# Performance work log

Hardware: AMD Instinct MI355X
Metric: run time of the kernel (lower is better)

Reference implementation:

```python
import jax, jax.numpy as jnp
import numpy as np

B, S, H, OUT = 512, 128, 512, 1
IN = 1
P = 0.1  # drop_rate


def setup_inputs() -> dict:
    key = jax.random.key(0)
    ks = jax.random.split(key, 14)
    x = jax.random.normal(ks[0], (B, S), dtype=jnp.float32)
    # Bayesian LSTM variational params (blitz-style: W = mu + log1p(exp(rho)) * eps)
    W_ih_mu = jax.random.normal(ks[1], (IN, 4 * H), dtype=jnp.float32) * 0.1
    W_ih_rho = jnp.full((IN, 4 * H), -5.0, dtype=jnp.float32)
    eps_ih = jax.random.normal(ks[2], (IN, 4 * H), dtype=jnp.float32)
    W_hh_mu = jax.random.normal(ks[3], (H, 4 * H), dtype=jnp.float32) * 0.1
    W_hh_rho = jnp.full((H, 4 * H), -5.0, dtype=jnp.float32)
    eps_hh = jax.random.normal(ks[4], (H, 4 * H), dtype=jnp.float32)
    b_mu = jax.random.normal(ks[5], (4 * H,), dtype=jnp.float32) * 0.1
    b_rho = jnp.full((4 * H,), -5.0, dtype=jnp.float32)
    eps_b = jax.random.normal(ks[6], (4 * H,), dtype=jnp.float32)
    # linear head
    W_lin = jax.random.normal(ks[7], (H, OUT), dtype=jnp.float32) * 0.05
    b_lin = jnp.zeros((OUT,), dtype=jnp.float32)
    # dropout masks (training=True always); pre-scaled inverted dropout
    keep = 1.0 - P
    mask_in = jax.random.bernoulli(ks[8], keep, (B, S, 1)).astype(jnp.float32) / keep
    # second dropout is applied to hidden_seq then sliced at t=-1, so only the
    # last-step mask matters
    mask_out = jax.random.bernoulli(ks[9], keep, (B, H)).astype(jnp.float32) / keep
    return {
        "x": x,
        "W_ih_mu": W_ih_mu, "W_ih_rho": W_ih_rho, "eps_ih": eps_ih,
        "W_hh_mu": W_hh_mu, "W_hh_rho": W_hh_rho, "eps_hh": eps_hh,
        "b_mu": b_mu, "b_rho": b_rho, "eps_b": eps_b,
        "W_lin": W_lin, "b_lin": b_lin,
        "mask_in": mask_in, "mask_out": mask_out,
    }


def reference(x, W_ih_mu, W_ih_rho, eps_ih, W_hh_mu, W_hh_rho, eps_hh,
              b_mu, b_rho, eps_b, W_lin, b_lin, mask_in, mask_out):
    # reparameterized weight samples
    W_ih = W_ih_mu + jnp.log1p(jnp.exp(W_ih_rho)) * eps_ih   # (IN, 4H)
    W_hh = W_hh_mu + jnp.log1p(jnp.exp(W_hh_rho)) * eps_hh   # (H, 4H)
    b = b_mu + jnp.log1p(jnp.exp(b_rho)) * eps_b             # (4H,)

    # reshape (B,S) -> (B,S,1) + input dropout
    xr = x[:, :, None] * mask_in                              # (B,S,1)
    # input projection for all timesteps at once
    x_proj = jnp.einsum('bsi,ih->bsh', xr, W_ih) + b          # (B,S,4H)
    xs = jnp.swapaxes(x_proj, 0, 1)                           # (S,B,4H)

    h0 = jnp.zeros((B, H), dtype=x.dtype)
    c0 = jnp.zeros((B, H), dtype=x.dtype)

    def step(carry, gx):
        h, c = carry
        gates = gx + h @ W_hh                                 # (B,4H)
        i_g, f_g, g_g, o_g = jnp.split(gates, 4, axis=-1)
        i_t = jax.nn.sigmoid(i_g)
        f_t = jax.nn.sigmoid(f_g)
        g_t = jnp.tanh(g_g)
        o_t = jax.nn.sigmoid(o_g)
        c_new = f_t * c + i_t * g_t
        h_new = o_t * jnp.tanh(c_new)
        return (h_new, c_new), h_new

    (h_last, _), _ = jax.lax.scan(step, (h0, c0), xs)
    # output dropout (only last step matters after slicing), then linear head
    out = (h_last * mask_out) @ W_lin + b_lin                 # (B,OUT)
    return out
```

## Files before the change

kernel.cpp:

```cpp
#include <hip/hip_runtime.h>
#include <hip/hip_bf16.h>


typedef __attribute__((ext_vector_type(8))) _Float16 half8;
typedef __attribute__((ext_vector_type(4))) float f32x4;
typedef unsigned long long u64;
typedef unsigned int u32;

#define HID   512
#define BATCH 512
#define SEQ   128

__device__ __forceinline__ float bf2f(__hip_bfloat16 v) { return __bfloat162float(v); }
__device__ __forceinline__ float softplus_f(float x) { return log1pf(__expf(x)); }
__device__ __forceinline__ float sigm(float x) { return 1.f / (1.f + __expf(-x)); }
__device__ __forceinline__ float tanh_fast(float x) {
  x = fminf(fmaxf(x, -15.f), 15.f);
  float e = __expf(2.f * x);
  return (e - 1.f) / (e + 1.f);
}
__device__ __forceinline__ float ldin(const void* p, size_t i, int md) {
  return md ? ((const float*)p)[i] : bf2f(((const __hip_bfloat16*)p)[i]);
}
__device__ __forceinline__ unsigned short f16bits(_Float16 h) {
  union { _Float16 f; unsigned short u; } c; c.f = h; return c.u;
}
__device__ __forceinline__ u64 ald64(const u64* p) {
  return __hip_atomic_load((u64*)p, __ATOMIC_RELAXED, __HIP_MEMORY_SCOPE_AGENT);
}
__device__ __forceinline__ u32 ald32(const u32* p) {
  return __hip_atomic_load((u32*)p, __ATOMIC_RELAXED, __HIP_MEMORY_SCOPE_AGENT);
}
__device__ __forceinline__ void ast32(u32* p, u32 v) {
  (void)__hip_atomic_exchange(p, v, __ATOMIC_RELAXED, __HIP_MEMORY_SCOPE_AGENT);
}
__device__ __forceinline__ void ast64(u64* p, u64 v) {
  (void)__hip_atomic_exchange(p, v, __ATOMIC_RELAXED, __HIP_MEMORY_SCOPE_AGENT);
}

__global__ void detect_mode(const u32* __restrict__ rho_bits, int* __restrict__ mode) {
  *mode = (rho_bits[0] == 0xC0A00000u) ? 1 : 0;
}

__global__ __launch_bounds__(256) void setup_weights(
    const void* __restrict__ mu, const void* __restrict__ rho,
    const void* __restrict__ eps, unsigned short* __restrict__ Wtf,
    const int* __restrict__ mode) {
  const int md = *mode;
  const int idx = blockIdx.x * 256 + threadIdx.x;
  const int k = idx >> 11, ncol = idx & 2047;
  const float w = ldin(mu, idx, md) + softplus_f(ldin(rho, idx, md)) * ldin(eps, idx, md);
  const int g = ncol >> 9, j = ncol & 511;
  const int js = j >> 4, rr = j & 15;
  const int kk = k >> 5, q = (k >> 3) & 3, slot = k & 7;
  const int lane = rr + 16 * q;
  const size_t off = ((size_t)((g * 32 + js) * 16 + kk) * 64 + lane) * 8 + slot;
  Wtf[off] = f16bits((_Float16)w);
}

__global__ void setup_misc(
    const void* __restrict__ x,
    const void* __restrict__ Wih_mu, const void* __restrict__ Wih_rho,
    const void* __restrict__ eps_ih,
    const void* __restrict__ b_mu, const void* __restrict__ b_rho,
    const void* __restrict__ eps_b,
    const void* __restrict__ mask_in,
    float* __restrict__ Wih4, float* __restrict__ bias4, float* __restrict__ xm,
    u32* __restrict__ hA32,
    u32* __restrict__ flags,
    const int* __restrict__ mode) {
  const int md = *mode;
  const int idx = blockIdx.x * blockDim.x + threadIdx.x;
  if (idx < 2048) {
    Wih4[idx] = ldin(Wih_mu, idx, md) + softplus_f(ldin(Wih_rho, idx, md)) * ldin(eps_ih, idx, md);
  } else if (idx < 4096) {
    const int n = idx - 2048;
    bias4[n] = ldin(b_mu, n, md) + softplus_f(ldin(b_rho, n, md)) * ldin(eps_b, n, md);
  } else if (idx < 69632) {
    const int i = idx - 4096;
    const int s = i >> 9, b = i & 511;
    const size_t src = (size_t)b * SEQ + s;
    xm[(size_t)s * BATCH + b] = ldin(x, src, md) * ldin(mask_in, src, md);
  } else if (idx < 200704) {
    hA32[idx - 69632] = 0u;
  } else if (idx < 204800) {
    flags[idx - 200704] = 0u;
  }
}

__global__ __launch_bounds__(512, 2) void lstm_persist(
    u64* __restrict__ hA, u64* __restrict__ hB,
    float* __restrict__ hf, const unsigned short* __restrict__ Wtf,
    const float* __restrict__ Wih4, const float* __restrict__ bias4,
    const float* __restrict__ xm, u32* __restrict__ flags) {
  __shared__ half8 WS[4096];
  __shared__ f32x4 exch[8][4][64];
  __shared__ u32 T[4][16][17];
  const int tid  = threadIdx.x;
  const int lane = tid & 63;
  const int wv   = tid >> 6;
  const int w    = wv & 3;
  const int hv   = wv >> 2;
  const int r = lane & 15, q = lane >> 4;
  const int bid = blockIdx.x;
  const int mg = bid >> 5, js = bid & 31;
  const int j0 = js * 16, m0 = mg * 64 + w * 16, mt = mg * 4 + w;

  for (int fi = tid; fi < 4096; fi += 512) {
    const int g  = fi >> 10;
    const int kk = (fi >> 6) & 15;
    const int ln = fi & 63;
    WS[fi] = *(const half8*)(Wtf + (((size_t)((g * 32 + js) * 16 + kk) * 64 + ln) * 8));
  }
  __syncthreads();

  const int jj = j0 + r;
  const float wih_i = Wih4[jj],             bi  = bias4[jj];
  const float wih_f = Wih4[HID + jj],       bfv = bias4[HID + jj];
  const float wih_g = Wih4[2 * HID + jj],   bg  = bias4[2 * HID + jj];
  const float wih_o = Wih4[3 * HID + jj],   bo  = bias4[3 * HID + jj];

  float cc0 = 0.f, cc1 = 0.f;
  u32* myflag = flags + (size_t)(mg * 32 + js) * 16;
  u32* pollp  = flags + (size_t)(mg * 32 + (lane & 31)) * 16;

  const int mtc = wv >> 1, half = wv & 1;
  const int sl = lane & 31;
  const int sri = sl & 15;
  const int sc0 = ((sl >> 4) << 3) + half * 4;
  const size_t oidx = (size_t)((mg * 4 + mtc) * 16 + (js >> 1)) * 128 +
                      (size_t)half * 64 + (size_t)(js & 1) * 32 + sl;

  for (int t = 0; t < SEQ; ++t) {
    const u64* ih = (t & 1) ? hB : hA;
    u64*       oh = (t & 1) ? hA : hB;

    const size_t rb = (size_t)(mt * 16 + hv * 8) * 128 + lane;
    u64 uh[16];
#pragma unroll
    for (int kkl = 0; kkl < 8; ++kkl) {
      uh[kkl * 2]     = ald64(ih + rb + (size_t)kkl * 128);
      uh[kkl * 2 + 1] = ald64(ih + rb + (size_t)kkl * 128 + 64);
    }

    const float xb0 = xm[t * BATCH + m0 + q * 4 + hv * 2 + 0];
    const float xb1 = xm[t * BATCH + m0 + q * 4 + hv * 2 + 1];

    f32x4 a0 = {0.f, 0.f, 0.f, 0.f};
    f32x4 a1 = a0, a2 = a0, a3 = a0;
#pragma unroll
    for (int kkl = 0; kkl < 8; ++kkl) {
      const int kk = hv * 8 + kkl;
      const half8 b0 = WS[(0 * 16 + kk) * 64 + lane];
      const half8 b1 = WS[(1 * 16 + kk) * 64 + lane];
      const half8 b2 = WS[(2 * 16 + kk) * 64 + lane];
      const half8 b3 = WS[(3 * 16 + kk) * 64 + lane];
      union { half8 h; u64 d[2]; } ah;
      ah.d[0] = uh[kkl * 2]; ah.d[1] = uh[kkl * 2 + 1];
      a0 = __builtin_amdgcn_mfma_f32_16x16x32_f16(ah.h, b0, a0, 0, 0, 0);
      a1 = __builtin_amdgcn_mfma_f32_16x16x32_f16(ah.h, b1, a1, 0, 0, 0);
      a2 = __builtin_amdgcn_mfma_f32_16x16x32_f16(ah.h, b2, a2, 0, 0, 0);
      a3 = __builtin_amdgcn_mfma_f32_16x16x32_f16(ah.h, b3, a3, 0, 0, 0);
    }

    exch[wv][0][lane] = a0; exch[wv][1][lane] = a1;
    exch[wv][2][lane] = a2; exch[wv][3][lane] = a3;
    __syncthreads();
    const int pw = wv ^ 4;
    a0 += exch[pw][0][lane]; a1 += exch[pw][1][lane];
    a2 += exch[pw][2][lane]; a3 += exch[pw][3][lane];

#pragma unroll
    for (int i2 = 0; i2 < 2; ++i2) {
      const int i = hv * 2 + i2;
      const int m = m0 + q * 4 + i;
      const float xb = i2 ? xb1 : xb0;
      const float pi = a0[i] + xb * wih_i + bi;
      const float pf = a1[i] + xb * wih_f + bfv;
      const float pg = a2[i] + xb * wih_g + bg;
      const float po = a3[i] + xb * wih_o + bo;
      const float cprev = i2 ? cc1 : cc0;
      const float cn = sigm(pf) * cprev + sigm(pi) * tanh_fast(pg);
      const float hn = sigm(po) * tanh_fast(cn);
      if (i2) cc1 = cn; else cc0 = cn;
      T[w][q * 4 + i][r] = (u32)f16bits((_Float16)hn);
      if (t == SEQ - 1) hf[(size_t)m * HID + jj] = hn;
    }
    __syncthreads();

    if (lane < 32) {
      const u32 x0 = T[mtc][sri][sc0];
      const u32 x1 = T[mtc][sri][sc0 + 1];
      const u32 x2 = T[mtc][sri][sc0 + 2];
      const u32 x3 = T[mtc][sri][sc0 + 3];
      const u64 hv64 = (u64)((x0 & 0xffffu) | (x1 << 16)) |
                       ((u64)((x2 & 0xffffu) | (x3 << 16)) << 32);
      ast64(oh + oidx, hv64);
    }

    if (t < SEQ - 1) {
      __syncthreads();
      if (tid == 0) ast32(myflag, (u32)(t + 1));
      const u32 tgt = (u32)(t + 1);
      long gd = 0;
      for (;;) {
        const u32 v = ald32(pollp);
        if (__ballot(v >= tgt) == ~0ULL) break;
        if (++gd > 50000000L) break;
      }
    }
  }
}

__global__ void head_kernel(const float* __restrict__ hf,
                            const void* __restrict__ mask_out,
                            const void* __restrict__ W_lin,
                            const void* __restrict__ b_lin,
                            void* __restrict__ out,
                            const int* __restrict__ mode) {
  const int md = *mode;
  const int b = blockIdx.x;
  const int lane = threadIdx.x;
  float s = 0.f;
#pragma unroll
  for (int j = lane; j < HID; j += 64) {
    s += hf[(size_t)b * HID + j] * ldin(mask_out, (size_t)b * HID + j, md) * ldin(W_lin, j, md);
  }
#pragma unroll
  for (int off = 32; off; off >>= 1) s += __shfl_down(s, off, 64);
  if (lane == 0) {
    const float v = s + ldin(b_lin, 0, md);
    if (md) ((float*)out)[b] = v;
    else    ((__hip_bfloat16*)out)[b] = __float2bfloat16(v);
  }
}

extern "C" void kernel_launch(void* const* d_in, const int* in_sizes, int n_in,
                              void* d_out, int out_size, void* d_ws, size_t ws_size,
                              hipStream_t stream) {
  const void* x        = d_in[0];
  const void* Wih_mu   = d_in[1];
  const void* Wih_rho  = d_in[2];
  const void* eps_ih   = d_in[3];
  const void* Whh_mu   = d_in[4];
  const void* Whh_rho  = d_in[5];
  const void* eps_hh   = d_in[6];
  const void* b_mu     = d_in[7];
  const void* b_rho    = d_in[8];
  const void* eps_b    = d_in[9];
  const void* W_lin    = d_in[10];
  const void* b_lin    = d_in[11];
  const void* mask_in  = d_in[12];
  const void* mask_out = d_in[13];

  char* ws = (char*)d_ws;
  unsigned short* Wtf = (unsigned short*)(ws);
  float* Wih4  = (float*)(ws + 2097152);
  float* bias4 = (float*)(ws + 2105344);
  float* xm    = (float*)(ws + 2113536);
  u64*   hA    = (u64*)(ws + 2375680);
  u64*   hB    = (u64*)(ws + 2899968);
  float* hf    = (float*)(ws + 3424256);
  u32*   flags = (u32*)(ws + 4472832);
  int*   mode  = (int*)(ws + 4489216);

  detect_mode<<<1, 1, 0, stream>>>((const u32*)b_rho, mode);
  setup_weights<<<4096, 256, 0, stream>>>(Whh_mu, Whh_rho, eps_hh, Wtf, mode);
  setup_misc<<<800, 256, 0, stream>>>(x, Wih_mu, Wih_rho, eps_ih, b_mu, b_rho, eps_b,
                                      mask_in, Wih4, bias4, xm,
                                      (u32*)hA, flags, mode);

  void* kargs[] = {&hA, &hB, &hf, &Wtf, &Wih4, &bias4, &xm, &flags};
  hipLaunchCooperativeKernel(reinterpret_cast<void*>(&lstm_persist),
                             dim3(256), dim3(512), kargs, 0, stream);

  head_kernel<<<BATCH, 64, 0, stream>>>(hf, mask_out, W_lin, b_lin, d_out, mode);
}
```

Before: 648.5 us.

## Split persistent LSTM into 512 small blocks without split-K reduction

```diff
diff --git a/kernel.cpp b/kernel.cpp
--- a/kernel.cpp
+++ b/kernel.cpp
@@ -83,30 +83,29 @@
     xm[(size_t)s * BATCH + b] = ldin(x, src, md) * ldin(mask_in, src, md);
   } else if (idx < 200704) {
     hA32[idx - 69632] = 0u;
-  } else if (idx < 204800) {
+  } else if (idx < 208896) {
     flags[idx - 200704] = 0u;
   }
 }
 
-__global__ __launch_bounds__(512, 2) void lstm_persist(
+__global__ __launch_bounds__(128, 2) void lstm_persist(
     u64* __restrict__ hA, u64* __restrict__ hB,
     float* __restrict__ hf, const unsigned short* __restrict__ Wtf,
     const float* __restrict__ Wih4, const float* __restrict__ bias4,
     const float* __restrict__ xm, u32* __restrict__ flags) {
   __shared__ half8 WS[4096];
-  __shared__ f32x4 exch[8][4][64];
-  __shared__ u32 T[4][16][17];
+  __shared__ u32 T[2][16][17];
   const int tid  = threadIdx.x;
   const int lane = tid & 63;
   const int wv   = tid >> 6;
-  const int w    = wv & 3;
-  const int hv   = wv >> 2;
   const int r = lane & 15, q = lane >> 4;
   const int bid = blockIdx.x;
   const int mg = bid >> 5, js = bid & 31;
-  const int j0 = js * 16, m0 = mg * 64 + w * 16, mt = mg * 4 + w;
-
-  for (int fi = tid; fi < 4096; fi += 512) {
+  const int j0 = js * 16;
+  const int mt = mg * 2 + wv;
+  const int m0 = mt * 16;
+
+  for (int fi = tid; fi < 4096; fi += 128) {
     const int g  = fi >> 10;
     const int kk = (fi >> 6) & 15;
     const int ln = fi & 63;
@@ -120,41 +119,37 @@
   const float wih_g = Wih4[2 * HID + jj],   bg  = bias4[2 * HID + jj];
   const float wih_o = Wih4[3 * HID + jj],   bo  = bias4[3 * HID + jj];
 
-  float cc0 = 0.f, cc1 = 0.f;
+  float cc[4] = {0.f, 0.f, 0.f, 0.f};
   u32* myflag = flags + (size_t)(mg * 32 + js) * 16;
   u32* pollp  = flags + (size_t)(mg * 32 + (lane & 31)) * 16;
 
-  const int mtc = wv >> 1, half = wv & 1;
+  const int half = lane >> 5;
   const int sl = lane & 31;
   const int sri = sl & 15;
   const int sc0 = ((sl >> 4) << 3) + half * 4;
-  const size_t oidx = (size_t)((mg * 4 + mtc) * 16 + (js >> 1)) * 128 +
+  const size_t oidx = (size_t)(mt * 16 + (js >> 1)) * 128 +
                       (size_t)half * 64 + (size_t)(js & 1) * 32 + sl;
 
   for (int t = 0; t < SEQ; ++t) {
     const u64* ih = (t & 1) ? hB : hA;
     u64*       oh = (t & 1) ? hA : hB;
 
-    const size_t rb = (size_t)(mt * 16 + hv * 8) * 128 + lane;
-    u64 uh[16];
-#pragma unroll
-    for (int kkl = 0; kkl < 8; ++kkl) {
+    const size_t rb = (size_t)(mt * 16) * 128 + lane;
+    u64 uh[32];
+#pragma unroll
+    for (int kkl = 0; kkl < 16; ++kkl) {
       uh[kkl * 2]     = ald64(ih + rb + (size_t)kkl * 128);
       uh[kkl * 2 + 1] = ald64(ih + rb + (size_t)kkl * 128 + 64);
     }
 
-    const float xb0 = xm[t * BATCH + m0 + q * 4 + hv * 2 + 0];
-    const float xb1 = xm[t * BATCH + m0 + q * 4 + hv * 2 + 1];
-
     f32x4 a0 = {0.f, 0.f, 0.f, 0.f};
     f32x4 a1 = a0, a2 = a0, a3 = a0;
 #pragma unroll
-    for (int kkl = 0; kkl < 8; ++kkl) {
-      const int kk = hv * 8 + kkl;
-      const half8 b0 = WS[(0 * 16 + kk) * 64 + lane];
-      const half8 b1 = WS[(1 * 16 + kk) * 64 + lane];
-      const half8 b2 = WS[(2 * 16 + kk) * 64 + lane];
-      const half8 b3 = WS[(3 * 16 + kk) * 64 + lane];
+    for (int kkl = 0; kkl < 16; ++kkl) {
+      const half8 b0 = WS[(0 * 16 + kkl) * 64 + lane];
+      const half8 b1 = WS[(1 * 16 + kkl) * 64 + lane];
+      const half8 b2 = WS[(2 * 16 + kkl) * 64 + lane];
+      const half8 b3 = WS[(3 * 16 + kkl) * 64 + lane];
       union { half8 h; u64 d[2]; } ah;
       ah.d[0] = uh[kkl * 2]; ah.d[1] = uh[kkl * 2 + 1];
       a0 = __builtin_amdgcn_mfma_f32_16x16x32_f16(ah.h, b0, a0, 0, 0, 0);
@@ -163,36 +158,27 @@
       a3 = __builtin_amdgcn_mfma_f32_16x16x32_f16(ah.h, b3, a3, 0, 0, 0);
     }
 
-    exch[wv][0][lane] = a0; exch[wv][1][lane] = a1;
-    exch[wv][2][lane] = a2; exch[wv][3][lane] = a3;
-    __syncthreads();
-    const int pw = wv ^ 4;
-    a0 += exch[pw][0][lane]; a1 += exch[pw][1][lane];
-    a2 += exch[pw][2][lane]; a3 += exch[pw][3][lane];
-
-#pragma unroll
-    for (int i2 = 0; i2 < 2; ++i2) {
-      const int i = hv * 2 + i2;
+#pragma unroll
+    for (int i = 0; i < 4; ++i) {
       const int m = m0 + q * 4 + i;
-      const float xb = i2 ? xb1 : xb0;
+      const float xb = xm[t * BATCH + m];
       const float pi = a0[i] + xb * wih_i + bi;
       const float pf = a1[i] + xb * wih_f + bfv;
       const float pg = a2[i] + xb * wih_g + bg;
       const float po = a3[i] + xb * wih_o + bo;
-      const float cprev = i2 ? cc1 : cc0;
-      const float cn = sigm(pf) * cprev + sigm(pi) * tanh_fast(pg);
+      const float cn = sigm(pf) * cc[i] + sigm(pi) * tanh_fast(pg);
       const float hn = sigm(po) * tanh_fast(cn);
-      if (i2) cc1 = cn; else cc0 = cn;
-      T[w][q * 4 + i][r] = (u32)f16bits((_Float16)hn);
+      cc[i] = cn;
+      T[wv][q * 4 + i][r] = (u32)f16bits((_Float16)hn);
       if (t == SEQ - 1) hf[(size_t)m * HID + jj] = hn;
     }
     __syncthreads();
 
-    if (lane < 32) {
-      const u32 x0 = T[mtc][sri][sc0];
-      const u32 x1 = T[mtc][sri][sc0 + 1];
-      const u32 x2 = T[mtc][sri][sc0 + 2];
-      const u32 x3 = T[mtc][sri][sc0 + 3];
+    {
+      const u32 x0 = T[wv][sri][sc0];
+      const u32 x1 = T[wv][sri][sc0 + 1];
+      const u32 x2 = T[wv][sri][sc0 + 2];
+      const u32 x3 = T[wv][sri][sc0 + 3];
       const u64 hv64 = (u64)((x0 & 0xffffu) | (x1 << 16)) |
                        ((u64)((x2 & 0xffffu) | (x3 << 16)) << 32);
       ast64(oh + oidx, hv64);
@@ -262,17 +248,17 @@
   u64*   hB    = (u64*)(ws + 2899968);
   float* hf    = (float*)(ws + 3424256);
   u32*   flags = (u32*)(ws + 4472832);
-  int*   mode  = (int*)(ws + 4489216);
+  int*   mode  = (int*)(ws + 4505600);
 
   detect_mode<<<1, 1, 0, stream>>>((const u32*)b_rho, mode);
   setup_weights<<<4096, 256, 0, stream>>>(Whh_mu, Whh_rho, eps_hh, Wtf, mode);
-  setup_misc<<<800, 256, 0, stream>>>(x, Wih_mu, Wih_rho, eps_ih, b_mu, b_rho, eps_b,
+  setup_misc<<<816, 256, 0, stream>>>(x, Wih_mu, Wih_rho, eps_ih, b_mu, b_rho, eps_b,
                                       mask_in, Wih4, bias4, xm,
                                       (u32*)hA, flags, mode);
 
   void* kargs[] = {&hA, &hB, &hf, &Wtf, &Wih4, &bias4, &xm, &flags};
   hipLaunchCooperativeKernel(reinterpret_cast<void*>(&lstm_persist),
-                             dim3(256), dim3(512), kargs, 0, stream);
+                             dim3(512), dim3(128), kargs, 0, stream);
 
   head_kernel<<<BATCH, 64, 0, stream>>>(hf, mask_out, W_lin, b_lin, d_out, mode);
 }
```

After: 792.9 us. 22.3% more time.
